# Optimization experiments

Measured on AMD Instinct MI355X. Metric: run time of the kernel, lower is better.

## Reference

```python
import jax, jax.numpy as jnp
import numpy as np

B, L, E, H = 32, 512, 1024, 1024


def setup_inputs() -> dict:
    key = jax.random.key(0)
    ks = jax.random.split(key, 12)
    s = 0.02
    return {
        "x": jax.random.normal(ks[0], (B, L, E), jnp.float32),
        "h0": jax.random.normal(ks[1], (B, L, H), jnp.float32),
        "c0": jax.random.normal(ks[2], (B, L, H), jnp.float32),
        "W_ioux": jax.random.normal(ks[3], (E, 3 * H), jnp.float32) * s,
        "W_iouh": jax.random.normal(ks[4], (2, H, 3 * H), jnp.float32) * s,
        "b_iouh": jax.random.normal(ks[5], (2, 3 * H), jnp.float32) * s,
        "W_fx": jax.random.normal(ks[6], (E, H), jnp.float32) * s,
        "W_fh": jax.random.normal(ks[7], (4, H, H), jnp.float32) * s,
        "b_fh": jax.random.normal(ks[8], (4, H), jnp.float32) * s,
        "tree_ids_d": jax.random.randint(ks[9], (B, L), 0, L, jnp.int32),
        "tree_ids_dr": jax.random.randint(ks[10], (B, L), 0, L, jnp.int32),
        "tree_ids_dl": jax.random.randint(ks[11], (B, L), 0, L, jnp.int32),
    }


def _scatter_add_rows(src, idx):
    # out[b, idx[b,l], :] += src[b, l, :]   (torch scatter_add_ on dim=1 with row-repeated index)
    b = jnp.arange(src.shape[0])[:, None]
    return jnp.zeros_like(src).at[b, idx].add(src)


def _gather_rows(src, idx):
    # out[b, l, :] = src[b, idx[b,l], :]    (torch gather on dim=1 with row-repeated index)
    return jnp.take_along_axis(src, idx[:, :, None], axis=1)


def _masked_scatter(dest, mask3, src):
    # torch masked_scatter_: True positions (flat order) filled with src elements in flat order
    mflat = mask3.reshape(-1)
    pos = jnp.cumsum(mflat.astype(jnp.int32)) - 1
    filled = jnp.take(src.reshape(-1), jnp.clip(pos, 0, src.size - 1))
    return jnp.where(mflat, filled, dest.reshape(-1)).reshape(dest.shape)


def reference(x, h0, c0, W_ioux, W_iouh, b_iouh, W_fx, W_fh, b_fh,
              tree_ids_d, tree_ids_dr, tree_ids_dl):
    Hh = h0.shape[-1]
    iou_x = x @ W_ioux                               # [B,L,3H]
    iou_hr = h0 @ W_iouh[0] + b_iouh[0]              # [B,L,3H]
    iou_hl = h0 @ W_iouh[1] + b_iouh[1]
    # original repeats index only to hidden_size -> only first H cols (i-gate) get scattered child states
    add = (_scatter_add_rows(iou_hr[..., :Hh], tree_ids_dr)
           + _scatter_add_rows(iou_hl[..., :Hh], tree_ids_dl))
    iou = iou_x.at[..., :Hh].add(add)
    i, o, u = jnp.split(iou, 3, axis=-1)
    i, o, u = jax.nn.sigmoid(i), jax.nn.sigmoid(o), jnp.tanh(u)

    fx = x @ W_fx                                    # [B,L,H]
    # fh[0],fh[1] both gathered at index_r; fh[2],fh[3] both at index_l -> fuse the GEMMs
    fr = h0 @ (W_fh[0] + W_fh[1]) + (b_fh[0] + b_fh[1])
    fl = h0 @ (W_fh[2] + W_fh[3]) + (b_fh[2] + b_fh[3])
    f = jax.nn.sigmoid(_gather_rows(fx, tree_ids_d)
                       + _gather_rows(fr, tree_ids_dr)
                       + _gather_rows(fl, tree_ids_dl))

    fc = f * c0
    c_new = i * u + _scatter_add_rows(fc, tree_ids_d)
    h_new = o * jnp.tanh(c_new)

    mask3 = jnp.broadcast_to((tree_ids_d != 0)[:, :, None], h_new.shape)
    h_out = _masked_scatter(h0, mask3, h_new)
    c_out = _masked_scatter(c0, mask3, c_new)
    return (h_out, c_out)
```

## Files before the change

kernel.cpp:

```cpp
#include <hip/hip_runtime.h>


#define ROWS 16384
#define HID  1024
#define KDIM 1024
#define NCOLS 4096
#define BM 256
#define BN 256
#define BK 64

typedef __attribute__((ext_vector_type(4))) int            i32x4;
typedef __attribute__((ext_vector_type(4))) float          f32x4;
typedef __attribute__((ext_vector_type(4))) unsigned short u16x4;

__device__ __forceinline__ unsigned short f2bf(float f) {
  unsigned u = __float_as_uint(f);
  unsigned r = 0x7FFFu + ((u >> 16) & 1u);
  return (unsigned short)((u + r) >> 16);
}
__device__ __forceinline__ float bf2f(unsigned short v) {
  return __uint_as_float(((unsigned)v) << 16);
}
__device__ __forceinline__ float sigmoidf_(float x) {
  return 1.0f / (1.0f + __expf(-x));
}
__device__ __forceinline__ void gload16(const void* g, void* l) {
  __builtin_amdgcn_global_load_lds(
      (const __attribute__((address_space(1))) void*)g,
      (__attribute__((address_space(3))) void*)l, 16, 0, 0);
}
__device__ __forceinline__ void mfma_bf16(f32x4& acc, i32x4 a, i32x4 b) {
  asm volatile("v_mfma_f32_16x16x32_bf16 %0, %1, %2, %0"
               : "+v"(acc) : "v"(a), "v"(b));
}


__global__ void pack_wx(const float* __restrict__ Wioux, const float* __restrict__ Wfx,
                        unsigned short* __restrict__ Wxt) {
  __shared__ float t[32][33];
  const int n0 = blockIdx.x * 32, k0 = blockIdx.y * 32;
  const int tx = threadIdx.x, ty = threadIdx.y;
  const int n = n0 + tx, k = k0 + ty;
  float v = (n < 3072) ? Wioux[(size_t)k * 3072 + n]
                       : Wfx[(size_t)k * 1024 + (n - 3072)];
  t[ty][tx] = v;
  __syncthreads();
  Wxt[(size_t)(n0 + ty) * KDIM + (k0 + tx)] = f2bf(t[tx][ty]);
}

__global__ void pack_wh(const float* __restrict__ Wiouh, const float* __restrict__ Wfh,
                        unsigned short* __restrict__ Wht) {
  __shared__ float t[32][33];
  const int n0 = blockIdx.x * 32, k0 = blockIdx.y * 32;
  const int tx = threadIdx.x, ty = threadIdx.y;
  const int n = n0 + tx, k = k0 + ty;
  float v;
  if (n < 1024)      v = Wiouh[(size_t)k * 3072 + n];
  else if (n < 2048) v = Wiouh[3145728u + (size_t)k * 3072 + (n - 1024)];
  else if (n < 3072) { const int c = n - 2048;
    v = Wfh[(size_t)k * 1024 + c] + Wfh[1048576u + (size_t)k * 1024 + c]; }
  else { const int c = n - 3072;
    v = Wfh[2097152u + (size_t)k * 1024 + c] + Wfh[3145728u + (size_t)k * 1024 + c]; }
  t[ty][tx] = v;
  __syncthreads();
  Wht[(size_t)(n0 + ty) * KDIM + (k0 + tx)] = f2bf(t[tx][ty]);
}

__global__ void pack_bias(const float* __restrict__ b_iouh, const float* __restrict__ b_fh,
                          float* __restrict__ bh) {
  const int n = blockIdx.x * 1024 + threadIdx.x;
  float v;
  if (n < 1024)      v = b_iouh[n];
  else if (n < 2048) v = b_iouh[3072 + (n - 1024)];
  else if (n < 3072) { const int c = n - 2048; v = b_fh[c] + b_fh[1024 + c]; }
  else { const int c = n - 3072; v = b_fh[2048 + c] + b_fh[3072 + c]; }
  bh[n] = v;
}

__global__ void convert_bf16(const float* __restrict__ x, const float* __restrict__ h0,
                             unsigned short* __restrict__ xb, unsigned short* __restrict__ hb) {
  const size_t i = ((size_t)blockIdx.x * 256 + threadIdx.x) * 4;
  const float4 a = *(const float4*)&x[i];
  const float4 b = *(const float4*)&h0[i];
  u16x4 av = { f2bf(a.x), f2bf(a.y), f2bf(a.z), f2bf(a.w) };
  u16x4 bv = { f2bf(b.x), f2bf(b.y), f2bf(b.z), f2bf(b.w) };
  *(u16x4*)&xb[i] = av;
  *(u16x4*)&hb[i] = bv;
}

__device__ __forceinline__ void stage8(const unsigned short* __restrict__ gp,
                                       unsigned short* __restrict__ lp,
                                       int rowbase, int gbase, int k0, int lane) {
  const int lrow = rowbase + (lane >> 3);
  const int sseg = (lane & 7) ^ ((lane >> 3) & 7);
  gload16(gp + (size_t)(gbase + lrow) * KDIM + k0 + sseg * 8,
          lp + ((size_t)rowbase << 6));
}

#define PHASE(qm, qn, STAGES, VM)                                            \
  {                                                                          \
    i32x4 af[4][2], bfr[2][2];                                               \
    const unsigned short* Ab = &S[b][0][0][0];                               \
    const unsigned short* Bb = &S[b][1][0][0];                               \
    _Pragma("unroll")                                                        \
    for (int i = 0; i < 4; ++i) {                                            \
      const int row = wr * 128 + (qm) * 64 + i * 16 + m0;                    \
      _Pragma("unroll")                                                      \
      for (int s = 0; s < 2; ++s)                                            \
        af[i][s] = *(const i32x4*)(Ab + row * 64 + (((kg + s * 4) ^ sw8) << 3)); \
    }                                                                        \
    _Pragma("unroll")                                                        \
    for (int j = 0; j < 2; ++j) {                                            \
      const int col = wc * 64 + (qn) * 32 + j * 16 + m0;                     \
      _Pragma("unroll")                                                      \
      for (int s = 0; s < 2; ++s)                                            \
        bfr[j][s] = *(const i32x4*)(Bb + col * 64 + (((kg + s * 4) ^ sw8) << 3)); \
    }                                                                        \
    STAGES;                                                                  \
    VM;                                                                      \
    __builtin_amdgcn_s_barrier();                                            \
    __builtin_amdgcn_s_setprio(1);                                           \
    _Pragma("unroll")                                                        \
    for (int i = 0; i < 4; ++i)                                              \
      _Pragma("unroll")                                                      \
      for (int j = 0; j < 2; ++j) {                                          \
        mfma_bf16(acc[(qm) * 4 + i][(qn) * 2 + j], af[i][0], bfr[j][0]);     \
        mfma_bf16(acc[(qm) * 4 + i][(qn) * 2 + j], af[i][1], bfr[j][1]);     \
      }                                                                      \
    __builtin_amdgcn_s_setprio(0);                                           \
    __builtin_amdgcn_s_barrier();                                            \
  }

__global__ __launch_bounds__(512, 2)
void gemm8(const unsigned short* __restrict__ xb, const unsigned short* __restrict__ hb,
           const unsigned short* __restrict__ Wxt, const unsigned short* __restrict__ Wht,
           unsigned short* __restrict__ gxb, unsigned short* __restrict__ ghb,
           const float* __restrict__ bhv) {
  __shared__ __align__(16) unsigned short S[2][2][256][64];

  const unsigned short* A;
  const unsigned short* Bt;
  unsigned short* Cp;
  const float* bias;
  if (blockIdx.z == 0) { A = xb; Bt = Wxt; Cp = gxb; bias = nullptr; }
  else                 { A = hb; Bt = Wht; Cp = ghb; bias = bhv; }

  const int tid = threadIdx.x, w = tid >> 6, lane = tid & 63;
  const int wr = w >> 2, wc = w & 3;
  const int bm = blockIdx.y * BM, bn = blockIdx.x * BN;
  const int m0 = lane & 15, kg = lane >> 4, sw8 = m0 & 7;
  const int bb0 = (w >> 2) * 64 + (w & 3) * 8;

  f32x4 acc[8][4] = {};

  stage8(A,  &S[0][0][0][0], w * 8,        bm, 0, lane);
  stage8(A,  &S[0][0][0][0], 128 + w * 8,  bm, 0, lane);
  stage8(A,  &S[0][0][0][0], 64 + w * 8,   bm, 0, lane);
  stage8(A,  &S[0][0][0][0], 192 + w * 8,  bm, 0, lane);
  stage8(Bt, &S[0][1][0][0], bb0,          bn, 0, lane);
  stage8(Bt, &S[0][1][0][0], bb0 + 128,    bn, 0, lane);
  stage8(Bt, &S[0][1][0][0], bb0 + 32,     bn, 0, lane);
  stage8(Bt, &S[0][1][0][0], bb0 + 160,    bn, 0, lane);
  asm volatile("s_waitcnt vmcnt(0)");
  __builtin_amdgcn_s_barrier();

  for (int t = 0; t < 16; ++t) {
    const int b = t & 1, nb = b ^ 1;
    const int k1 = (t + 1) << 6;
    const bool st = (t < 15);
    unsigned short* An = &S[nb][0][0][0];
    unsigned short* Bn = &S[nb][1][0][0];

    PHASE(0, 0,
      { if (st) { stage8(A, An, w * 8, bm, k1, lane);
                  stage8(A, An, 128 + w * 8, bm, k1, lane); } },
      {});
    PHASE(0, 1,
      { if (st) { stage8(Bt, Bn, bb0, bn, k1, lane);
                  stage8(Bt, Bn, bb0 + 128, bn, k1, lane); } },
      { if (st) asm volatile("s_waitcnt vmcnt(4)");
        else    asm volatile("s_waitcnt vmcnt(0)"); });
    PHASE(1, 0,
      { if (st) { stage8(Bt, Bn, bb0 + 32, bn, k1, lane);
                  stage8(Bt, Bn, bb0 + 160, bn, k1, lane); } },
      {});
    PHASE(1, 1,
      { if (st) { stage8(A, An, 64 + w * 8, bm, k1, lane);
                  stage8(A, An, 192 + w * 8, bm, k1, lane); } },
      { asm volatile("s_waitcnt vmcnt(2)"); });
  }

  const int rg = kg * 4;
#pragma unroll
  for (int mi = 0; mi < 8; ++mi) {
#pragma unroll
    for (int nj = 0; nj < 4; ++nj) {
      const int col = bn + wc * 64 + nj * 16 + m0;
      const float bv = bias ? bias[col] : 0.0f;
      const int row = bm + wr * 128 + mi * 16 + rg;
#pragma unroll
      for (int r = 0; r < 4; ++r)
        Cp[(size_t)(row + r) * NCOLS + col] = f2bf(acc[mi][nj][r] + bv);
    }
  }
}

__global__ void scan_mask(const int* __restrict__ idd, int* __restrict__ sel,
                          int* __restrict__ mcount) {
  __shared__ int ps[1024];
  const int t = threadIdx.x;
  int loc[16];
  int cnt = 0;
#pragma unroll
  for (int i = 0; i < 16; ++i) {
    const int v = (idd[t * 16 + i] != 0) ? 1 : 0;
    loc[i] = v; cnt += v;
  }
  ps[t] = cnt;
  __syncthreads();
  for (int off = 1; off < 1024; off <<= 1) {
    const int add = (t >= off) ? ps[t - off] : 0;
    __syncthreads();
    ps[t] += add;
    __syncthreads();
  }
  int rank = (t == 0) ? 0 : ps[t - 1];
#pragma unroll
  for (int i = 0; i < 16; ++i)
    if (loc[i]) sel[rank++] = t * 16 + i;
  if (t == 1023) *mcount = ps[1023];
}

__global__ void build_csr(const int* __restrict__ idd, const int* __restrict__ idr,
                          const int* __restrict__ idl,
                          int* __restrict__ ofsD, int* __restrict__ ofsR, int* __restrict__ ofsL,
                          int* __restrict__ lstD, int* __restrict__ lstR, int* __restrict__ lstL) {
  __shared__ int sidx[512];
  __shared__ int scan[512];
  const int b = blockIdx.x, t = threadIdx.x;
  const int gb = b << 9;
  const int* const srcs[3] = { idd, idr, idl };
  int* const ofss[3] = { ofsD, ofsR, ofsL };
  int* const lsts[3] = { lstD, lstR, lstL };
  for (int a = 0; a < 3; ++a) {
    sidx[t] = srcs[a][gb + t];
    scan[t] = 0;
    __syncthreads();
    atomicAdd(&scan[sidx[t]], 1);
    __syncthreads();
    int v = scan[t];
    for (int off = 1; off < 512; off <<= 1) {
      const int add = (t >= off) ? scan[t - off] : 0;
      __syncthreads();
      scan[t] += add;
      __syncthreads();
    }
    const int start = scan[t] - v;
    ofss[a][b * 513 + t] = start;
    if (t == 511) ofss[a][b * 513 + 512] = scan[511];
    int pos = start;
    for (int l = 0; l < 512; ++l)
      if (sidx[l] == t) lsts[a][gb + (pos++)] = l;
    __syncthreads();
  }
}

__global__ __launch_bounds__(256)
void fused_final(const unsigned short* __restrict__ gxb, const unsigned short* __restrict__ ghb,
                 const float* __restrict__ h0, const float* __restrict__ c0,
                 const int* __restrict__ idd, const int* __restrict__ idr,
                 const int* __restrict__ idl,
                 const int* __restrict__ ofsR, const int* __restrict__ lstR,
                 const int* __restrict__ ofsL, const int* __restrict__ lstL,
                 const int* __restrict__ ofsD, const int* __restrict__ lstD,
                 const int* __restrict__ sel, const int* __restrict__ mcount,
                 float* __restrict__ hout, float* __restrict__ cout, int r0) {
  const int r = blockIdx.x;
  const int g = r0 + r;
  const int j = g & 511;
  const int bb = g >> 9;
  const int lbase = (r >> 9) << 9;
  const int ob = bb * 513;
  const int lb = bb << 9;
  const int c = threadIdx.x << 2;

  float a0 = 0.f, a1 = 0.f, a2 = 0.f, a3 = 0.f;
  for (int q = ofsR[ob + j], e = ofsR[ob + j + 1]; q < e; ++q) {
    const int l = lstR[lb + q];
    const u16x4 v = *(const u16x4*)&ghb[(size_t)(lbase + l) * NCOLS + c];
    a0 += bf2f(v[0]); a1 += bf2f(v[1]); a2 += bf2f(v[2]); a3 += bf2f(v[3]);
  }
  for (int q = ofsL[ob + j], e = ofsL[ob + j + 1]; q < e; ++q) {
    const int l = lstL[lb + q];
    const u16x4 v = *(const u16x4*)&ghb[(size_t)(lbase + l) * NCOLS + 1024 + c];
    a0 += bf2f(v[0]); a1 += bf2f(v[1]); a2 += bf2f(v[2]); a3 += bf2f(v[3]);
  }

  const u16x4 fx4 = *(const u16x4*)&gxb[(size_t)r * NCOLS + 3072 + c];
  const float fx0 = bf2f(fx4[0]), fx1 = bf2f(fx4[1]), fx2 = bf2f(fx4[2]), fx3 = bf2f(fx4[3]);
  float fc0 = 0.f, fc1 = 0.f, fc2 = 0.f, fc3 = 0.f;
  for (int q = ofsD[ob + j], e = ofsD[ob + j + 1]; q < e; ++q) {
    const int l = lstD[lb + q];
    const int jr = idr[lb + l], jl = idl[lb + l];
    const u16x4 rv = *(const u16x4*)&ghb[(size_t)(lbase + jr) * NCOLS + 2048 + c];
    const u16x4 lv = *(const u16x4*)&ghb[(size_t)(lbase + jl) * NCOLS + 3072 + c];
    const float4 cc = *(const float4*)&c0[(size_t)(lb + l) * HID + c];
    fc0 += sigmoidf_(fx0 + bf2f(rv[0]) + bf2f(lv[0])) * cc.x;
    fc1 += sigmoidf_(fx1 + bf2f(rv[1]) + bf2f(lv[1])) * cc.y;
    fc2 += sigmoidf_(fx2 + bf2f(rv[2]) + bf2f(lv[2])) * cc.z;
    fc3 += sigmoidf_(fx3 + bf2f(rv[3]) + bf2f(lv[3])) * cc.w;
  }

  const u16x4 vi = *(const u16x4*)&gxb[(size_t)r * NCOLS + c];
  const u16x4 vo = *(const u16x4*)&gxb[(size_t)r * NCOLS + 1024 + c];
  const u16x4 vu = *(const u16x4*)&gxb[(size_t)r * NCOLS + 2048 + c];
  float4 hn, cn;
  {
    const float ig = sigmoidf_(bf2f(vi[0]) + a0), og = sigmoidf_(bf2f(vo[0]));
    cn.x = ig * tanhf(bf2f(vu[0])) + fc0; hn.x = og * tanhf(cn.x);
  }
  {
    const float ig = sigmoidf_(bf2f(vi[1]) + a1), og = sigmoidf_(bf2f(vo[1]));
    cn.y = ig * tanhf(bf2f(vu[1])) + fc1; hn.y = og * tanhf(cn.y);
  }
  {
    const float ig = sigmoidf_(bf2f(vi[2]) + a2), og = sigmoidf_(bf2f(vo[2]));
    cn.z = ig * tanhf(bf2f(vu[2])) + fc2; hn.z = og * tanhf(cn.z);
  }
  {
    const float ig = sigmoidf_(bf2f(vi[3]) + a3), og = sigmoidf_(bf2f(vo[3]));
    cn.w = ig * tanhf(bf2f(vu[3])) + fc3; hn.w = og * tanhf(cn.w);
  }

  if (idd[g] == 0) {
    *(float4*)&hout[(size_t)g * HID + c] = *(const float4*)&h0[(size_t)g * HID + c];
    *(float4*)&cout[(size_t)g * HID + c] = *(const float4*)&c0[(size_t)g * HID + c];
  }
  const int m = *mcount;
  if (g < m) {
    const int o = sel[g];
    *(float4*)&hout[(size_t)o * HID + c] = hn;
    *(float4*)&cout[(size_t)o * HID + c] = cn;
  }
}

extern "C" void kernel_launch(void* const* d_in, const int* in_sizes, int n_in,
                              void* d_out, int out_size, void* d_ws, size_t ws_size,
                              hipStream_t stream) {
  const float* x      = (const float*)d_in[0];
  const float* h0     = (const float*)d_in[1];
  const float* c0     = (const float*)d_in[2];
  const float* W_ioux = (const float*)d_in[3];
  const float* W_iouh = (const float*)d_in[4];
  const float* b_iouh = (const float*)d_in[5];
  const float* W_fx   = (const float*)d_in[6];
  const float* W_fh   = (const float*)d_in[7];
  const float* b_fh   = (const float*)d_in[8];
  const int* idd      = (const int*)d_in[9];
  const int* idr      = (const int*)d_in[10];
  const int* idl      = (const int*)d_in[11];
  float* hout = (float*)d_out;
  float* cout = hout + (size_t)ROWS * HID;

  char* ws = (char*)d_ws;
  unsigned short* Wxt  = (unsigned short*)(ws);
  unsigned short* Wht  = (unsigned short*)(ws + 8388608u);
  float*          bh   = (float*)(ws + 16777216u);
  int*            sel  = (int*)(ws + 16793600u);
  int*            mcnt = (int*)(ws + 16859136u);
  int*            ofsD = (int*)(ws + 16859392u);
  int*            ofsR = (int*)(ws + 16925184u);
  int*            ofsL = (int*)(ws + 16990976u);
  int*            lstD = (int*)(ws + 17056768u);
  int*            lstR = (int*)(ws + 17122304u);
  int*            lstL = (int*)(ws + 17187840u);
  const size_t    base = 17253376u;

  int C = 32;
  while (C > 1 && base + 10485760ull * (size_t)C > ws_size) C >>= 1;
  const int R = 512 * C;

  char* p = ws + base;
  unsigned short* xb  = (unsigned short*)p;  p += 1048576ull * C;
  unsigned short* hb  = (unsigned short*)p;  p += 1048576ull * C;
  unsigned short* gxb = (unsigned short*)p;  p += 4194304ull * C;
  unsigned short* ghb = (unsigned short*)p;

  pack_wx<<<dim3(128, 32), dim3(32, 32), 0, stream>>>(W_ioux, W_fx, Wxt);
  pack_wh<<<dim3(128, 32), dim3(32, 32), 0, stream>>>(W_iouh, W_fh, Wht);
  pack_bias<<<4, 1024, 0, stream>>>(b_iouh, b_fh, bh);
  scan_mask<<<1, 1024, 0, stream>>>(idd, sel, mcnt);
  build_csr<<<32, 512, 0, stream>>>(idd, idr, idl, ofsD, ofsR, ofsL, lstD, lstR, lstL);

  for (int b0 = 0; b0 < 32; b0 += C) {
    const size_t r0 = (size_t)b0 * 512;
    convert_bf16<<<R, 256, 0, stream>>>(x + r0 * HID, h0 + r0 * HID, xb, hb);
    gemm8<<<dim3(NCOLS / BN, R / BM, 2), 512, 0, stream>>>(xb, hb, Wxt, Wht, gxb, ghb, bh);
    fused_final<<<R, 256, 0, stream>>>(gxb, ghb, h0, c0, idd, idr, idl,
                                       ofsR, lstR, ofsL, lstL, ofsD, lstD,
                                       sel, mcnt, hout, cout, (int)r0);
  }
}
```

Measured before the change: 552.8 us.

## Restructure GEMM main loop into two phases and remap blocks across XCDs

Replaces the four-phase interleaved load/MFMA schedule with a two-phase loop. All next-tile global loads are issued up front, each phase reuses the B fragments over 64 rows of A, and the wait for loads is a single vmcnt(0) before the second phase. It also remaps block indices so that consecutive blocks, which hardware spreads across the 8 XCDs, get grouped by M-chunk per XCD to improve L2 reuse. The cost is fewer barriers but less fine-grained overlap, plus more fragment registers live at once, which may pressure occupancy at 2 blocks per CU.

```diff
diff --git a/kernel.cpp b/kernel.cpp
--- a/kernel.cpp
+++ b/kernel.cpp
@@ -97,40 +97,6 @@
           lp + ((size_t)rowbase << 6));
 }
 
-#define PHASE(qm, qn, STAGES, VM)                                            \
-  {                                                                          \
-    i32x4 af[4][2], bfr[2][2];                                               \
-    const unsigned short* Ab = &S[b][0][0][0];                               \
-    const unsigned short* Bb = &S[b][1][0][0];                               \
-    _Pragma("unroll")                                                        \
-    for (int i = 0; i < 4; ++i) {                                            \
-      const int row = wr * 128 + (qm) * 64 + i * 16 + m0;                    \
-      _Pragma("unroll")                                                      \
-      for (int s = 0; s < 2; ++s)                                            \
-        af[i][s] = *(const i32x4*)(Ab + row * 64 + (((kg + s * 4) ^ sw8) << 3)); \
-    }                                                                        \
-    _Pragma("unroll")                                                        \
-    for (int j = 0; j < 2; ++j) {                                            \
-      const int col = wc * 64 + (qn) * 32 + j * 16 + m0;                     \
-      _Pragma("unroll")                                                      \
-      for (int s = 0; s < 2; ++s)                                            \
-        bfr[j][s] = *(const i32x4*)(Bb + col * 64 + (((kg + s * 4) ^ sw8) << 3)); \
-    }                                                                        \
-    STAGES;                                                                  \
-    VM;                                                                      \
-    __builtin_amdgcn_s_barrier();                                            \
-    __builtin_amdgcn_s_setprio(1);                                           \
-    _Pragma("unroll")                                                        \
-    for (int i = 0; i < 4; ++i)                                              \
-      _Pragma("unroll")                                                      \
-      for (int j = 0; j < 2; ++j) {                                          \
-        mfma_bf16(acc[(qm) * 4 + i][(qn) * 2 + j], af[i][0], bfr[j][0]);     \
-        mfma_bf16(acc[(qm) * 4 + i][(qn) * 2 + j], af[i][1], bfr[j][1]);     \
-      }                                                                      \
-    __builtin_amdgcn_s_setprio(0);                                           \
-    __builtin_amdgcn_s_barrier();                                            \
-  }
-
 __global__ __launch_bounds__(512, 2)
 void gemm8(const unsigned short* __restrict__ xb, const unsigned short* __restrict__ hb,
            const unsigned short* __restrict__ Wxt, const unsigned short* __restrict__ Wht,
@@ -145,21 +111,31 @@
   if (blockIdx.z == 0) { A = xb; Bt = Wxt; Cp = gxb; bias = nullptr; }
   else                 { A = hb; Bt = Wht; Cp = ghb; bias = bhv; }
 
+  int bx = blockIdx.x, by = blockIdx.y;
+  const int ny = gridDim.y;
+  if ((ny & 7) == 0) {
+    const int n = blockIdx.x + 16 * blockIdx.y;
+    const int xcd = n & 7, idx = n >> 3;
+    const int ych = ny >> 3;
+    bx = idx / ych;
+    by = xcd * ych + (idx % ych);
+  }
+  const int bm = by * BM, bn = bx * BN;
+
   const int tid = threadIdx.x, w = tid >> 6, lane = tid & 63;
   const int wr = w >> 2, wc = w & 3;
-  const int bm = blockIdx.y * BM, bn = blockIdx.x * BN;
   const int m0 = lane & 15, kg = lane >> 4, sw8 = m0 & 7;
-  const int bb0 = (w >> 2) * 64 + (w & 3) * 8;
+  const int bb0 = wr * 64 + wc * 8;
 
   f32x4 acc[8][4] = {};
 
   stage8(A,  &S[0][0][0][0], w * 8,        bm, 0, lane);
+  stage8(A,  &S[0][0][0][0], 64 + w * 8,   bm, 0, lane);
   stage8(A,  &S[0][0][0][0], 128 + w * 8,  bm, 0, lane);
-  stage8(A,  &S[0][0][0][0], 64 + w * 8,   bm, 0, lane);
   stage8(A,  &S[0][0][0][0], 192 + w * 8,  bm, 0, lane);
   stage8(Bt, &S[0][1][0][0], bb0,          bn, 0, lane);
+  stage8(Bt, &S[0][1][0][0], bb0 + 32,     bn, 0, lane);
   stage8(Bt, &S[0][1][0][0], bb0 + 128,    bn, 0, lane);
-  stage8(Bt, &S[0][1][0][0], bb0 + 32,     bn, 0, lane);
   stage8(Bt, &S[0][1][0][0], bb0 + 160,    bn, 0, lane);
   asm volatile("s_waitcnt vmcnt(0)");
   __builtin_amdgcn_s_barrier();
@@ -170,24 +146,65 @@
     const bool st = (t < 15);
     unsigned short* An = &S[nb][0][0][0];
     unsigned short* Bn = &S[nb][1][0][0];
-
-    PHASE(0, 0,
-      { if (st) { stage8(A, An, w * 8, bm, k1, lane);
-                  stage8(A, An, 128 + w * 8, bm, k1, lane); } },
-      {});
-    PHASE(0, 1,
-      { if (st) { stage8(Bt, Bn, bb0, bn, k1, lane);
-                  stage8(Bt, Bn, bb0 + 128, bn, k1, lane); } },
-      { if (st) asm volatile("s_waitcnt vmcnt(4)");
-        else    asm volatile("s_waitcnt vmcnt(0)"); });
-    PHASE(1, 0,
-      { if (st) { stage8(Bt, Bn, bb0 + 32, bn, k1, lane);
-                  stage8(Bt, Bn, bb0 + 160, bn, k1, lane); } },
-      {});
-    PHASE(1, 1,
-      { if (st) { stage8(A, An, 64 + w * 8, bm, k1, lane);
-                  stage8(A, An, 192 + w * 8, bm, k1, lane); } },
-      { asm volatile("s_waitcnt vmcnt(2)"); });
+    const unsigned short* Ab = &S[b][0][0][0];
+    const unsigned short* Bb = &S[b][1][0][0];
+
+    if (st) {
+      stage8(A,  An, w * 8,        bm, k1, lane);
+      stage8(A,  An, 64 + w * 8,   bm, k1, lane);
+      stage8(A,  An, 128 + w * 8,  bm, k1, lane);
+      stage8(A,  An, 192 + w * 8,  bm, k1, lane);
+      stage8(Bt, Bn, bb0,          bn, k1, lane);
+      stage8(Bt, Bn, bb0 + 32,     bn, k1, lane);
+      stage8(Bt, Bn, bb0 + 128,    bn, k1, lane);
+      stage8(Bt, Bn, bb0 + 160,    bn, k1, lane);
+    }
+    i32x4 af[4][2], bfr[4][2];
+#pragma unroll
+    for (int i = 0; i < 4; ++i) {
+      const int row = wr * 128 + i * 16 + m0;
+#pragma unroll
+      for (int s = 0; s < 2; ++s)
+        af[i][s] = *(const i32x4*)(Ab + row * 64 + (((kg + s * 4) ^ sw8) << 3));
+    }
+#pragma unroll
+    for (int jj = 0; jj < 4; ++jj) {
+      const int col = wc * 64 + jj * 16 + m0;
+#pragma unroll
+      for (int s = 0; s < 2; ++s)
+        bfr[jj][s] = *(const i32x4*)(Bb + col * 64 + (((kg + s * 4) ^ sw8) << 3));
+    }
+    __builtin_amdgcn_s_barrier();
+    __builtin_amdgcn_s_setprio(1);
+#pragma unroll
+    for (int i = 0; i < 4; ++i)
+#pragma unroll
+      for (int jj = 0; jj < 4; ++jj) {
+        mfma_bf16(acc[i][jj], af[i][0], bfr[jj][0]);
+        mfma_bf16(acc[i][jj], af[i][1], bfr[jj][1]);
+      }
+    __builtin_amdgcn_s_setprio(0);
+    __builtin_amdgcn_s_barrier();
+
+#pragma unroll
+    for (int i = 0; i < 4; ++i) {
+      const int row = wr * 128 + 64 + i * 16 + m0;
+#pragma unroll
+      for (int s = 0; s < 2; ++s)
+        af[i][s] = *(const i32x4*)(Ab + row * 64 + (((kg + s * 4) ^ sw8) << 3));
+    }
+    asm volatile("s_waitcnt vmcnt(0)");
+    __builtin_amdgcn_s_barrier();
+    __builtin_amdgcn_s_setprio(1);
+#pragma unroll
+    for (int i = 0; i < 4; ++i)
+#pragma unroll
+      for (int jj = 0; jj < 4; ++jj) {
+        mfma_bf16(acc[4 + i][jj], af[i][0], bfr[jj][0]);
+        mfma_bf16(acc[4 + i][jj], af[i][1], bfr[jj][1]);
+      }
+    __builtin_amdgcn_s_setprio(0);
+    __builtin_amdgcn_s_barrier();
   }
 
   const int rg = kg * 4;
```

Measured after the change: 573.3 us. +3.7%, slower.
